# Performance work log

Measured on AMD Instinct MI355X. Metric: run time of the kernel, lower is better.

Reference implementation:

```python
import jax, jax.numpy as jnp
import numpy as np

B, S, T = 32, 2048, 768
NH, DH, DHID = 8, 96, 384  # num_heads, head_dim, hidden_dim=4*head_dim


def setup_inputs() -> dict:
    key = jax.random.key(0)
    k = jax.random.split(key, 7)
    token_embeddings = jax.random.normal(k[0], (B, S, T), dtype=jnp.float32)
    attention_mask = jnp.ones((B, S), dtype=jnp.float32)
    # per-head Linear params, stacked on a leading head axis (PyTorch default-ish init scale)
    P_w = jax.random.normal(k[1], (NH, T, DH), dtype=jnp.float32) * (1.0 / np.sqrt(T))
    P_b = jax.random.normal(k[2], (NH, DH), dtype=jnp.float32) * 0.01
    W1_w = jax.random.normal(k[3], (NH, DH, DHID), dtype=jnp.float32) * (1.0 / np.sqrt(DH))
    W1_b = jax.random.normal(k[4], (NH, DHID), dtype=jnp.float32) * 0.01
    W2_w = jax.random.normal(k[5], (NH, DHID, DH), dtype=jnp.float32) * (1.0 / np.sqrt(DHID))
    W2_b = jax.random.normal(k[6], (NH, DH), dtype=jnp.float32) * 0.01
    return {
        'token_embeddings': token_embeddings,
        'attention_mask': attention_mask,
        'P_w': P_w, 'P_b': P_b,
        'W1_w': W1_w, 'W1_b': W1_b,
        'W2_w': W2_w, 'W2_b': W2_b,
    }


def reference(token_embeddings, attention_mask, P_w, P_b, W1_w, W1_b, W2_w, W2_b):
    # Batched over heads instead of the original Python loop; same math per head.
    # H_i = P_i(H): (B, NH, S, DH)
    Hi = jnp.einsum('bst,htd->bhsd', token_embeddings, P_w) + P_b[None, :, None, :]
    # A_i = W2_i(relu(W1_i(H_i))): (B, NH, S, DH)
    A = jax.nn.relu(jnp.einsum('bhsd,hde->bhse', Hi, W1_w) + W1_b[None, :, None, :])
    A = jnp.einsum('bhse,hed->bhsd', A, W2_w) + W2_b[None, :, None, :]
    # masked softmax over the sequence axis (log(mask) adds -inf at padded tokens)
    log_mask = jnp.log(attention_mask)[:, None, :, None]  # (B,1,S,1)
    A = jax.nn.softmax(A + log_mask, axis=2)
    # weighted sum over tokens: (B, NH, DH)
    v = jnp.sum(Hi * A, axis=2)
    # concat heads -> (B, NH*DH) == (B, sentence_dim)
    return v.reshape(v.shape[0], NH * DH)
```

## Files before the change

kernel.cpp:

```cpp
#include <hip/hip_runtime.h>
#include <cstdint>
#include <cstddef>

#define Bsz   32
#define Ssz   2048
#define Tsz   768
#define NH    8
#define DH    96
#define DHID  384
#define Ncols (NH*DH)

using u16 = unsigned short;
typedef __bf16 bf16x8 __attribute__((ext_vector_type(8)));
typedef __bf16 bf16x4 __attribute__((ext_vector_type(4)));
typedef float  f32x4  __attribute__((ext_vector_type(4)));

__device__ __forceinline__ u16 f2bn(float f) {
  __bf16 h = (__bf16)f;
  return __builtin_bit_cast(u16, h);
}
__device__ __forceinline__ float b2f(u16 u) {
  return __builtin_bit_cast(float, (uint32_t)u << 16);
}

__global__ __launch_bounds__(256) void k_pack(const float* __restrict__ Pw,
    const float* __restrict__ W1w, const float* __restrict__ W2w,
    u16* __restrict__ B1t, u16* __restrict__ W1t, u16* __restrict__ W2t)
{
  int i = blockIdx.x * 256 + threadIdx.x;
  if (i < 589824) {
    int n = i / 768, k = i % 768;
    int h = n / 96, d = n % 96;
    B1t[i] = f2bn(Pw[(size_t)h*73728 + (size_t)k*96 + d]);
  } else if (i < 589824 + 294912) {
    int j = i - 589824;
    int h = j / 36864, r = j % 36864;
    int n = r / 96, k = r % 96;
    W1t[j] = f2bn(W1w[(size_t)h*36864 + (size_t)k*384 + n]);
  } else if (i < 589824 + 2*294912) {
    int q = i - 589824 - 294912;
    int h = q / 36864, r = q % 36864;
    int n = r / 384, k = r % 384;
    W2t[q] = f2bn(W2w[(size_t)h*36864 + (size_t)k*96 + n]);
  }
}

__global__ __launch_bounds__(256, 2) void k_gemm1(const float* __restrict__ emb,
    const u16* __restrict__ B1t, const float* __restrict__ Pb, u16* __restrict__ Hi)
{
  __shared__ u16 As[2][128*64];
  __shared__ u16 Bs[2][128*64];
  const int tid  = threadIdx.x;
  const int lane = tid & 63;
  const int w    = tid >> 6;
  const int wr = w >> 1, wc = w & 1;
  const int L = blockIdx.x;
  const int widx = (L & 7) * 384 + (L >> 3);
  const int bm = widx / 6, bn = widx % 6;
  const int l15 = lane & 15, lg = lane >> 4;

  const int srow   = lane >> 3;
  const int schunk = lane & 7;
  const int wchunk = schunk ^ srow;

  bf16x8 pa[4];
  bf16x8 pb[4];

  auto load_tile = [&](int kt) {
    const int k0 = kt * 64;
    #pragma unroll
    for (int i = 0; i < 4; ++i) {
      const int row = w*32 + i*8 + srow;
      const float* src = emb + (size_t)(bm*128 + row)*Tsz + k0 + schunk*8;
      float4 v0 = *reinterpret_cast<const float4*>(src);
      float4 v1 = *reinterpret_cast<const float4*>(src + 4);
      bf16x8 af;
      af[0] = (__bf16)v0.x; af[1] = (__bf16)v0.y; af[2] = (__bf16)v0.z; af[3] = (__bf16)v0.w;
      af[4] = (__bf16)v1.x; af[5] = (__bf16)v1.y; af[6] = (__bf16)v1.z; af[7] = (__bf16)v1.w;
      pa[i] = af;
    }
    #pragma unroll
    for (int i = 0; i < 4; ++i) {
      const int row = w*32 + i*8 + srow;
      pb[i] = *reinterpret_cast<const bf16x8*>(
          B1t + (size_t)(bn*128 + row)*Tsz + k0 + schunk*8);
    }
  };
  auto write_tile = [&](int buf) {
    #pragma unroll
    for (int i = 0; i < 4; ++i) {
      const int row = w*32 + i*8 + srow;
      *reinterpret_cast<bf16x8*>(&As[buf][row*64 + wchunk*8]) = pa[i];
      *reinterpret_cast<bf16x8*>(&Bs[buf][row*64 + wchunk*8]) = pb[i];
    }
  };

  f32x4 acc[4][4] = {};

  load_tile(0);
  write_tile(0);
  __syncthreads();

  #pragma unroll 1
  for (int kt = 0; kt < 12; ++kt) {
    const int cur = kt & 1;
    if (kt < 11) load_tile(kt + 1);
    __builtin_amdgcn_s_setprio(1);
    #pragma unroll
    for (int kk = 0; kk < 2; ++kk) {
      const int clog = kk*4 + lg;
      bf16x8 b[4];
      #pragma unroll
      for (int c = 0; c < 4; ++c) {
        const int Rb = wc*64 + c*16 + l15;
        b[c] = *reinterpret_cast<const bf16x8*>(&Bs[cur][Rb*64 + (clog ^ (Rb & 7))*8]);
      }
      bf16x8 a[4];
      #pragma unroll
      for (int m = 0; m < 4; ++m) {
        const int R = wr*64 + m*16 + l15;
        a[m] = *reinterpret_cast<const bf16x8*>(&As[cur][R*64 + (clog ^ (R & 7))*8]);
      }
      #pragma unroll
      for (int m = 0; m < 4; ++m)
        #pragma unroll
        for (int c = 0; c < 4; ++c)
          acc[m][c] = __builtin_amdgcn_mfma_f32_16x16x32_bf16(a[m], b[c], acc[m][c], 0, 0, 0);
    }
    __builtin_amdgcn_s_setprio(0);
    if (kt < 11) write_tile(cur ^ 1);
    __syncthreads();
  }

  #pragma unroll
  for (int c = 0; c < 4; ++c) {
    int col = bn*128 + wc*64 + c*16 + l15;
    float bias = Pb[col];
    #pragma unroll
    for (int m = 0; m < 4; ++m) {
      int row0 = bm*128 + wr*64 + m*16 + lg*4;
      #pragma unroll
      for (int j = 0; j < 4; ++j)
        Hi[(size_t)(row0 + j)*Ncols + col] = f2bn(acc[m][c][j] + bias);
    }
  }
}

__global__ __launch_bounds__(256, 1) void k_ffn_pool(
    const u16* __restrict__ Hi, const u16* __restrict__ W1t, const u16* __restrict__ W2t,
    const float* __restrict__ b1, const float* __restrict__ b2v, const float* __restrict__ mask,
    float* __restrict__ out)
{
  __shared__ u16 W1s[384][104];
  __shared__ u16 W2s[96][392];
  __shared__ u16 Zb[4][16][40];

  const int tid = threadIdx.x, lane = tid & 63, w = tid >> 6;
  const int l15 = lane & 15, lg = lane >> 4;
  const int h = blockIdx.x, b = blockIdx.y;

  const u16* W1h = W1t + (size_t)h * DHID * DH;
  const u16* W2h = W2t + (size_t)h * DH * DHID;
  const float* b1h = b1 + h * DHID;

  for (int i = tid; i < 384*12; i += 256) {
    int r = i / 12, g = i % 12;
    uint4 v = *reinterpret_cast<const uint4*>(W1h + (size_t)r*DH + g*8);
    *reinterpret_cast<uint4*>(&W1s[r][g*8]) = v;
  }
  for (int i = tid; i < 96*48; i += 256) {
    int r = i / 48, g = i % 48;
    uint4 v = *reinterpret_cast<const uint4*>(W2h + (size_t)r*DHID + g*8);
    *reinterpret_cast<uint4*>(&W2s[r][g*8]) = v;
  }
  __syncthreads();

  float b2s[6];
  #pragma unroll
  for (int ct = 0; ct < 6; ++ct) b2s[ct] = b2v[h*DH + ct*16 + l15];

  float Mr[6], Lr[6], Ar[6];
  #pragma unroll
  for (int ct = 0; ct < 6; ++ct) { Mr[ct] = -3.4e38f; Lr[ct] = 0.f; Ar[ct] = 0.f; }

  #pragma unroll 1
  for (int pass = 0; pass < 8; ++pass) {
    const size_t prow = (size_t)b*Ssz + (size_t)w*512 + (size_t)pass*64;

    bf16x8 hifr[4][3];
    #pragma unroll
    for (int s = 0; s < 4; ++s)
      #pragma unroll
      for (int ks = 0; ks < 3; ++ks)
        hifr[s][ks] = *reinterpret_cast<const bf16x8*>(
            Hi + (prow + s*16 + l15)*Ncols + h*DH + ks*32 + lg*8);

    f32x4 lgt[4][6] = {};

    #pragma unroll 2
    for (int c = 0; c < 12; ++c) {
      bf16x8 a1c[2][3];
      #pragma unroll
      for (int t = 0; t < 2; ++t)
        #pragma unroll
        for (int ks = 0; ks < 3; ++ks)
          a1c[t][ks] = *reinterpret_cast<const bf16x8*>(
              &W1s[c*32 + t*16 + l15][ks*32 + lg*8]);
      float4 bc0 = *reinterpret_cast<const float4*>(b1h + c*32 + lg*4);
      float4 bc1 = *reinterpret_cast<const float4*>(b1h + c*32 + 16 + lg*4);
      bf16x8 b2fr[6];
      #pragma unroll
      for (int ct = 0; ct < 6; ++ct)
        b2fr[ct] = *reinterpret_cast<const bf16x8*>(&W2s[ct*16 + l15][c*32 + lg*8]);

      #pragma unroll
      for (int s = 0; s < 4; ++s) {
        f32x4 z0 = {}, z1 = {};
        #pragma unroll
        for (int ks = 0; ks < 3; ++ks) {
          z0 = __builtin_amdgcn_mfma_f32_16x16x32_bf16(a1c[0][ks], hifr[s][ks], z0, 0, 0, 0);
          z1 = __builtin_amdgcn_mfma_f32_16x16x32_bf16(a1c[1][ks], hifr[s][ks], z1, 0, 0, 0);
        }
        bf16x4 p0, p1;
        p0[0] = (__bf16)fmaxf(z0[0] + bc0.x, 0.f);
        p0[1] = (__bf16)fmaxf(z0[1] + bc0.y, 0.f);
        p0[2] = (__bf16)fmaxf(z0[2] + bc0.z, 0.f);
        p0[3] = (__bf16)fmaxf(z0[3] + bc0.w, 0.f);
        p1[0] = (__bf16)fmaxf(z1[0] + bc1.x, 0.f);
        p1[1] = (__bf16)fmaxf(z1[1] + bc1.y, 0.f);
        p1[2] = (__bf16)fmaxf(z1[2] + bc1.z, 0.f);
        p1[3] = (__bf16)fmaxf(z1[3] + bc1.w, 0.f);
        *reinterpret_cast<uint2*>(&Zb[w][l15][lg*4])      = __builtin_bit_cast(uint2, p0);
        *reinterpret_cast<uint2*>(&Zb[w][l15][16 + lg*4]) = __builtin_bit_cast(uint2, p1);
        bf16x8 zf = *reinterpret_cast<const bf16x8*>(&Zb[w][l15][lg*8]);
        #pragma unroll
        for (int ct = 0; ct < 6; ++ct)
          lgt[s][ct] = __builtin_amdgcn_mfma_f32_16x16x32_bf16(zf, b2fr[ct], lgt[s][ct], 0, 0, 0);
      }
    }

    float lmv[4][4];
    #pragma unroll
    for (int s = 0; s < 4; ++s) {
      float4 mk = *reinterpret_cast<const float4*>(&mask[prow + s*16 + lg*4]);
      lmv[s][0] = __logf(mk.x); lmv[s][1] = __logf(mk.y);
      lmv[s][2] = __logf(mk.z); lmv[s][3] = __logf(mk.w);
    }
    float G[4][6][4];
    #pragma unroll
    for (int s = 0; s < 4; ++s)
      #pragma unroll
      for (int ct = 0; ct < 6; ++ct)
        #pragma unroll
        for (int j = 0; j < 4; ++j)
          G[s][ct][j] = b2f(Hi[(prow + s*16 + lg*4 + j)*Ncols + h*DH + ct*16 + l15]);

    #pragma unroll
    for (int ct = 0; ct < 6; ++ct) {
      float av[4][4];
      float m16 = -3.4e38f;
      #pragma unroll
      for (int s = 0; s < 4; ++s)
        #pragma unroll
        for (int j = 0; j < 4; ++j) {
          av[s][j] = lgt[s][ct][j] + b2s[ct] + lmv[s][j];
          m16 = fmaxf(m16, av[s][j]);
        }
      m16 = fmaxf(m16, __shfl_xor(m16, 16));
      m16 = fmaxf(m16, __shfl_xor(m16, 32));
      float l16 = 0.f, a16 = 0.f;
      #pragma unroll
      for (int s = 0; s < 4; ++s)
        #pragma unroll
        for (int j = 0; j < 4; ++j) {
          float p = __expf(av[s][j] - m16);
          l16 += p;
          a16 += p * G[s][ct][j];
        }
      l16 += __shfl_xor(l16, 16); l16 += __shfl_xor(l16, 32);
      a16 += __shfl_xor(a16, 16); a16 += __shfl_xor(a16, 32);
      float M2 = fmaxf(Mr[ct], m16);
      float eo = __expf(Mr[ct] - M2), en = __expf(m16 - M2);
      Lr[ct] = Lr[ct]*eo + l16*en;
      Ar[ct] = Ar[ct]*eo + a16*en;
      Mr[ct] = M2;
    }
  }

  float* mw = reinterpret_cast<float*>(&Zb[w][0][0]);
  if (lane < 16) {
    #pragma unroll
    for (int ct = 0; ct < 6; ++ct) {
      mw[      ct*16 + l15] = Mr[ct];
      mw[ 96 + ct*16 + l15] = Lr[ct];
      mw[192 + ct*16 + l15] = Ar[ct];
    }
  }
  __syncthreads();
  if (tid < 96) {
    const float* m0 = reinterpret_cast<const float*>(&Zb[0][0][0]);
    const float* m1 = reinterpret_cast<const float*>(&Zb[1][0][0]);
    const float* m2 = reinterpret_cast<const float*>(&Zb[2][0][0]);
    const float* m3 = reinterpret_cast<const float*>(&Zb[3][0][0]);
    float m = fmaxf(fmaxf(m0[tid], m1[tid]), fmaxf(m2[tid], m3[tid]));
    float e0 = __expf(m0[tid] - m), e1 = __expf(m1[tid] - m);
    float e2 = __expf(m2[tid] - m), e3 = __expf(m3[tid] - m);
    float l = m0[96+tid]*e0 + m1[96+tid]*e1 + m2[96+tid]*e2 + m3[96+tid]*e3;
    float a = m0[192+tid]*e0 + m1[192+tid]*e1 + m2[192+tid]*e2 + m3[192+tid]*e3;
    out[(size_t)b * Ncols + h*DH + tid] = a / l;
  }
}

extern "C" void kernel_launch(void* const* d_in, const int* in_sizes, int n_in,
                              void* d_out, int out_size, void* d_ws, size_t ws_size,
                              hipStream_t stream)
{
  const float* emb  = (const float*)d_in[0];
  const float* mask = (const float*)d_in[1];
  const float* Pw   = (const float*)d_in[2];
  const float* Pb   = (const float*)d_in[3];
  const float* W1w  = (const float*)d_in[4];
  const float* W1b  = (const float*)d_in[5];
  const float* W2w  = (const float*)d_in[6];
  const float* W2b  = (const float*)d_in[7];
  float* out = (float*)d_out;

  char* ws = (char*)d_ws;
  u16*   Hi  = (u16*)(ws);
  u16*   B1t = (u16*)(ws + 100663296ull);
  u16*   W1t = (u16*)(ws + 101842944ull);
  u16*   W2t = (u16*)(ws + 102432768ull);

  k_pack<<<dim3(4608), dim3(256), 0, stream>>>(Pw, W1w, W2w, B1t, W1t, W2t);
  k_gemm1<<<dim3(3072), dim3(256), 0, stream>>>(emb, B1t, Pb, Hi);
  k_ffn_pool<<<dim3(8, 32), dim3(256), 0, stream>>>(Hi, W1t, W2t, W1b, W2b, mask, out);
}
```

Measured before the change: 265.9 us.

## Load GEMM1 fragments directly from global memory, dropping LDS staging

```diff
diff --git a/kernel.cpp b/kernel.cpp
--- a/kernel.cpp
+++ b/kernel.cpp
@@ -45,11 +45,9 @@
   }
 }
 
-__global__ __launch_bounds__(256, 2) void k_gemm1(const float* __restrict__ emb,
+__global__ __launch_bounds__(256) void k_gemm1(const float* __restrict__ emb,
     const u16* __restrict__ B1t, const float* __restrict__ Pb, u16* __restrict__ Hi)
 {
-  __shared__ u16 As[2][128*64];
-  __shared__ u16 Bs[2][128*64];
   const int tid  = threadIdx.x;
   const int lane = tid & 63;
   const int w    = tid >> 6;
@@ -59,77 +57,44 @@
   const int bm = widx / 6, bn = widx % 6;
   const int l15 = lane & 15, lg = lane >> 4;
 
-  const int srow   = lane >> 3;
-  const int schunk = lane & 7;
-  const int wchunk = schunk ^ srow;
-
-  bf16x8 pa[4];
-  bf16x8 pb[4];
-
-  auto load_tile = [&](int kt) {
-    const int k0 = kt * 64;
-    #pragma unroll
-    for (int i = 0; i < 4; ++i) {
-      const int row = w*32 + i*8 + srow;
-      const float* src = emb + (size_t)(bm*128 + row)*Tsz + k0 + schunk*8;
-      float4 v0 = *reinterpret_cast<const float4*>(src);
-      float4 v1 = *reinterpret_cast<const float4*>(src + 4);
-      bf16x8 af;
-      af[0] = (__bf16)v0.x; af[1] = (__bf16)v0.y; af[2] = (__bf16)v0.z; af[3] = (__bf16)v0.w;
-      af[4] = (__bf16)v1.x; af[5] = (__bf16)v1.y; af[6] = (__bf16)v1.z; af[7] = (__bf16)v1.w;
-      pa[i] = af;
-    }
-    #pragma unroll
-    for (int i = 0; i < 4; ++i) {
-      const int row = w*32 + i*8 + srow;
-      pb[i] = *reinterpret_cast<const bf16x8*>(
-          B1t + (size_t)(bn*128 + row)*Tsz + k0 + schunk*8);
-    }
-  };
-  auto write_tile = [&](int buf) {
-    #pragma unroll
-    for (int i = 0; i < 4; ++i) {
-      const int row = w*32 + i*8 + srow;
-      *reinterpret_cast<bf16x8*>(&As[buf][row*64 + wchunk*8]) = pa[i];
-      *reinterpret_cast<bf16x8*>(&Bs[buf][row*64 + wchunk*8]) = pb[i];
-    }
-  };
+  const float* aBase[4];
+  const u16*   bBase[4];
+  #pragma unroll
+  for (int m = 0; m < 4; ++m)
+    aBase[m] = emb + (size_t)(bm*128 + wr*64 + m*16 + l15) * Tsz + lg*8;
+  #pragma unroll
+  for (int c = 0; c < 4; ++c)
+    bBase[c] = B1t + (size_t)(bn*128 + wc*64 + c*16 + l15) * Tsz + lg*8;
 
   f32x4 acc[4][4] = {};
-
-  load_tile(0);
-  write_tile(0);
-  __syncthreads();
 
   #pragma unroll 1
   for (int kt = 0; kt < 12; ++kt) {
-    const int cur = kt & 1;
-    if (kt < 11) load_tile(kt + 1);
-    __builtin_amdgcn_s_setprio(1);
     #pragma unroll
     for (int kk = 0; kk < 2; ++kk) {
-      const int clog = kk*4 + lg;
+      const int kO = kt*64 + kk*32;
       bf16x8 b[4];
       #pragma unroll
-      for (int c = 0; c < 4; ++c) {
-        const int Rb = wc*64 + c*16 + l15;
-        b[c] = *reinterpret_cast<const bf16x8*>(&Bs[cur][Rb*64 + (clog ^ (Rb & 7))*8]);
+      for (int c = 0; c < 4; ++c)
+        b[c] = *reinterpret_cast<const bf16x8*>(bBase[c] + kO);
+      bf16x8 a[4];
+      #pragma unroll
+      for (int m = 0; m < 4; ++m) {
+        float4 v0 = *reinterpret_cast<const float4*>(aBase[m] + kO);
+        float4 v1 = *reinterpret_cast<const float4*>(aBase[m] + kO + 4);
+        bf16x8 af;
+        af[0] = (__bf16)v0.x; af[1] = (__bf16)v0.y; af[2] = (__bf16)v0.z; af[3] = (__bf16)v0.w;
+        af[4] = (__bf16)v1.x; af[5] = (__bf16)v1.y; af[6] = (__bf16)v1.z; af[7] = (__bf16)v1.w;
+        a[m] = af;
       }
-      bf16x8 a[4];
-      #pragma unroll
-      for (int m = 0; m < 4; ++m) {
-        const int R = wr*64 + m*16 + l15;
-        a[m] = *reinterpret_cast<const bf16x8*>(&As[cur][R*64 + (clog ^ (R & 7))*8]);
-      }
+      __builtin_amdgcn_s_setprio(1);
       #pragma unroll
       for (int m = 0; m < 4; ++m)
         #pragma unroll
         for (int c = 0; c < 4; ++c)
           acc[m][c] = __builtin_amdgcn_mfma_f32_16x16x32_bf16(a[m], b[c], acc[m][c], 0, 0, 0);
-    }
-    __builtin_amdgcn_s_setprio(0);
-    if (kt < 11) write_tile(cur ^ 1);
-    __syncthreads();
+      __builtin_amdgcn_s_setprio(0);
+    }
   }
 
   #pragma unroll
```

New measurement: 520.9 us. +95.9%, slower.

## Pre-convert embeddings to bf16 and load GEMM tiles via global_load_lds

Applied to the files above, without the earlier changes.

```diff
diff --git a/kernel.cpp b/kernel.cpp
--- a/kernel.cpp
+++ b/kernel.cpp
@@ -21,6 +21,28 @@
 }
 __device__ __forceinline__ float b2f(u16 u) {
   return __builtin_bit_cast(float, (uint32_t)u << 16);
+}
+
+typedef const __attribute__((address_space(1))) void* gas_t;
+typedef __attribute__((address_space(3))) void* las_t;
+__device__ __forceinline__ void gload16(const void* g, void* s) {
+  __builtin_amdgcn_global_load_lds((gas_t)g, (las_t)s, 16, 0, 0);
+}
+
+__global__ __launch_bounds__(256) void k_cvt(const float* __restrict__ e,
+                                             u16* __restrict__ o)
+{
+  size_t t = (size_t)blockIdx.x * 256 + threadIdx.x;
+  #pragma unroll
+  for (int it = 0; it < 3; ++it) {
+    size_t i = (t + (size_t)it * 2097152) * 8;
+    float4 v0 = *reinterpret_cast<const float4*>(e + i);
+    float4 v1 = *reinterpret_cast<const float4*>(e + i + 4);
+    bf16x8 p;
+    p[0] = (__bf16)v0.x; p[1] = (__bf16)v0.y; p[2] = (__bf16)v0.z; p[3] = (__bf16)v0.w;
+    p[4] = (__bf16)v1.x; p[5] = (__bf16)v1.y; p[6] = (__bf16)v1.z; p[7] = (__bf16)v1.w;
+    *reinterpret_cast<bf16x8*>(o + i) = p;
+  }
 }
 
 __global__ __launch_bounds__(256) void k_pack(const float* __restrict__ Pw,
@@ -45,7 +67,79 @@
   }
 }
 
-__global__ __launch_bounds__(256, 2) void k_gemm1(const float* __restrict__ emb,
+__global__ __launch_bounds__(256) void k_gemm1(const u16* __restrict__ embb,
+    const u16* __restrict__ B1t, const float* __restrict__ Pb, u16* __restrict__ Hi)
+{
+  __shared__ u16 As[128*64];
+  __shared__ u16 Bs[128*64];
+  const int tid  = threadIdx.x;
+  const int lane = tid & 63;
+  const int w    = tid >> 6;
+  const int wr = w >> 1, wc = w & 1;
+  const int L = blockIdx.x;
+  const int widx = (L & 7) * 384 + (L >> 3);
+  const int bm = widx / 6, bn = widx % 6;
+  const int l15 = lane & 15, lg = lane >> 4;
+
+  const int lrow = lane >> 3;
+  const int lchk = (lane & 7) ^ lrow;
+
+  f32x4 acc[4][4] = {};
+
+  #pragma unroll 1
+  for (int kt = 0; kt < 12; ++kt) {
+    const int k0 = kt * 64;
+    #pragma unroll
+    for (int i = 0; i < 4; ++i) {
+      const int r8 = (w*4 + i)*8;
+      gload16(embb + (size_t)(bm*128 + r8 + lrow)*Tsz + k0 + lchk*8,
+              &As[r8*64]);
+      gload16(B1t  + (size_t)(bn*128 + r8 + lrow)*Tsz + k0 + lchk*8,
+              &Bs[r8*64]);
+    }
+    __syncthreads();
+
+    __builtin_amdgcn_s_setprio(1);
+    #pragma unroll
+    for (int kk = 0; kk < 2; ++kk) {
+      const int clog = kk*4 + lg;
+      bf16x8 b[4];
+      #pragma unroll
+      for (int c = 0; c < 4; ++c) {
+        const int Rb = wc*64 + c*16 + l15;
+        b[c] = *reinterpret_cast<const bf16x8*>(&Bs[Rb*64 + (clog ^ (Rb & 7))*8]);
+      }
+      bf16x8 a[4];
+      #pragma unroll
+      for (int m = 0; m < 4; ++m) {
+        const int R = wr*64 + m*16 + l15;
+        a[m] = *reinterpret_cast<const bf16x8*>(&As[R*64 + (clog ^ (R & 7))*8]);
+      }
+      #pragma unroll
+      for (int m = 0; m < 4; ++m)
+        #pragma unroll
+        for (int c = 0; c < 4; ++c)
+          acc[m][c] = __builtin_amdgcn_mfma_f32_16x16x32_bf16(a[m], b[c], acc[m][c], 0, 0, 0);
+    }
+    __builtin_amdgcn_s_setprio(0);
+    __syncthreads();
+  }
+
+  #pragma unroll
+  for (int c = 0; c < 4; ++c) {
+    int col = bn*128 + wc*64 + c*16 + l15;
+    float bias = Pb[col];
+    #pragma unroll
+    for (int m = 0; m < 4; ++m) {
+      int row0 = bm*128 + wr*64 + m*16 + lg*4;
+      #pragma unroll
+      for (int j = 0; j < 4; ++j)
+        Hi[(size_t)(row0 + j)*Ncols + col] = f2bn(acc[m][c][j] + bias);
+    }
+  }
+}
+
+__global__ __launch_bounds__(256, 2) void k_gemm1_fb(const float* __restrict__ emb,
     const u16* __restrict__ B1t, const float* __restrict__ Pb, u16* __restrict__ Hi)
 {
   __shared__ u16 As[2][128*64];
@@ -326,12 +420,23 @@
   float* out = (float*)d_out;
 
   char* ws = (char*)d_ws;
-  u16*   Hi  = (u16*)(ws);
-  u16*   B1t = (u16*)(ws + 100663296ull);
-  u16*   W1t = (u16*)(ws + 101842944ull);
-  u16*   W2t = (u16*)(ws + 102432768ull);
-
-  k_pack<<<dim3(4608), dim3(256), 0, stream>>>(Pw, W1w, W2w, B1t, W1t, W2t);
-  k_gemm1<<<dim3(3072), dim3(256), 0, stream>>>(emb, B1t, Pb, Hi);
-  k_ffn_pool<<<dim3(8, 32), dim3(256), 0, stream>>>(Hi, W1t, W2t, W1b, W2b, mask, out);
-}
+  if (ws_size >= 203685888ull) {
+    u16* embb = (u16*)(ws);
+    u16* Hi   = (u16*)(ws + 100663296ull);
+    u16* B1t  = (u16*)(ws + 201326592ull);
+    u16* W1t  = (u16*)(ws + 202506240ull);
+    u16* W2t  = (u16*)(ws + 203096064ull);
+    k_cvt <<<dim3(8192), dim3(256), 0, stream>>>(emb, embb);
+    k_pack<<<dim3(4608), dim3(256), 0, stream>>>(Pw, W1w, W2w, B1t, W1t, W2t);
+    k_gemm1<<<dim3(3072), dim3(256), 0, stream>>>(embb, B1t, Pb, Hi);
+    k_ffn_pool<<<dim3(8, 32), dim3(256), 0, stream>>>(Hi, W1t, W2t, W1b, W2b, mask, out);
+  } else {
+    u16* Hi  = (u16*)(ws);
+    u16* B1t = (u16*)(ws + 100663296ull);
+    u16* W1t = (u16*)(ws + 101842944ull);
+    u16* W2t = (u16*)(ws + 102432768ull);
+    k_pack<<<dim3(4608), dim3(256), 0, stream>>>(Pw, W1w, W2w, B1t, W1t, W2t);
+    k_gemm1_fb<<<dim3(3072), dim3(256), 0, stream>>>(emb, B1t, Pb, Hi);
+    k_ffn_pool<<<dim3(8, 32), dim3(256), 0, stream>>>(Hi, W1t, W2t, W1b, W2b, mask, out);
+  }
+}
```

Result: slower. 286.0 us (+7.5%).
